# Kernel optimization log

Measured on AMD Instinct MI355X. Metric: run time of the kernel, lower is better.

## Reference

```python
import jax, jax.numpy as jnp
import numpy as np

MIN_NORM = 1e-15
BALL_EPS = 4e-3  # float32 proj eps used by HGCN PoincareBall
C_IN = 1.0
C_OUT = 1.0
N_NODES = 100000
N_EDGES = 1200000
DIM = 64
RATIO = 0.75


def _artanh(x):
    x = jnp.clip(x, -1.0 + 1e-7, 1.0 - 1e-7)
    return 0.5 * (jnp.log1p(x) - jnp.log1p(-x))


def _norm(x):
    return jnp.clip(jnp.linalg.norm(x, axis=-1, keepdims=True), MIN_NORM, None)


def proj(x, c):
    n = _norm(x)
    maxnorm = (1.0 - BALL_EPS) / jnp.sqrt(c)
    return jnp.where(n > maxnorm, x / n * maxnorm, x)


def expmap0(u, c):
    sc = jnp.sqrt(c)
    n = _norm(u)
    return jnp.tanh(sc * n) * u / (sc * n)


def logmap0(p, c):
    sc = jnp.sqrt(c)
    n = _norm(p)
    return _artanh(sc * n) * p / (sc * n)


def mobius_add(x, y, c):
    x2 = jnp.sum(x * x, -1, keepdims=True)
    y2 = jnp.sum(y * y, -1, keepdims=True)
    xy = jnp.sum(x * y, -1, keepdims=True)
    num = (1.0 + 2.0 * c * xy + c * y2) * x + (1.0 - c * x2) * y
    den = 1.0 + 2.0 * c * xy + c * c * x2 * y2
    return num / jnp.clip(den, MIN_NORM, None)


def mobius_matvec(m, x, c):
    sc = jnp.sqrt(c)
    xn = _norm(x)
    mx = x @ m.T  # [N, out]
    mxn = _norm(mx)
    res = jnp.tanh(mxn / xn * _artanh(sc * xn)) * mx / (mxn * sc)
    zero = jnp.all(mx == 0, axis=-1, keepdims=True)
    return jnp.where(zero, jnp.zeros((), mx.dtype), res)


def setup_inputs() -> dict:
    key = jax.random.key(0)
    k1, k2, k3, k4 = jax.random.split(key, 4)
    # points on the Poincare ball (small tangent vectors exp-mapped)
    x = proj(expmap0(0.01 * jax.random.normal(k1, (N_NODES, DIM), jnp.float32), C_IN), C_IN)
    edge_index = jax.random.randint(k2, (2, N_EDGES), 0, N_NODES, dtype=jnp.int32)
    xav = float(np.sqrt(2.0) * np.sqrt(6.0 / (DIM + DIM)))  # xavier_uniform gain sqrt(2) scale
    weight = jax.random.uniform(k3, (DIM, DIM), jnp.float32, -xav, xav)
    bias = jnp.zeros((DIM,), jnp.float32)
    lw_w = jax.random.normal(k4, (1, 2 * DIM), jnp.float32) * 0.05
    lw_b = jnp.zeros((1,), jnp.float32)
    return {"x": x, "edge_index": edge_index, "weight": weight, "bias": bias, "lw_w": lw_w, "lw_b": lw_b}


def reference(x, edge_index, weight, bias, lw_w, lw_b):
    N = x.shape[0]
    # ---- HypLinear (eval mode, dropout=0) ----
    h = proj(mobius_matvec(weight, x, C_IN), C_IN)
    hyp_bias = proj(expmap0(bias[None, :], C_IN), C_IN)  # proj_tan0 is identity on Poincare ball
    h = proj(mobius_add(h, hyp_bias, C_IN), C_IN)
    # ---- NodeSelect ----
    x_tan = logmap0(h, C_IN)  # [N, D]
    src, dst = edge_index[0], edge_index[1]
    agg = lambda v: jax.ops.segment_sum(v[src], dst, num_segments=N)  # scatter-add over edges
    sum_neigh = agg(x_tan)
    # NodeInformationScore: (I - D^{-1/2} A D^{-1/2}) x with self-loops removed from A
    w = (src != dst).astype(x_tan.dtype)
    deg = jax.ops.segment_sum(w, src, num_segments=N)
    dinv = jnp.where(deg > 0, deg ** -0.5, 0.0)
    norm_w = -(dinv[src] * w * dinv[dst])  # [E]
    info = x_tan + jax.ops.segment_sum(norm_w[:, None] * x_tan[src], dst, num_segments=N)
    score = jnp.sum(jnp.abs(info), axis=1)  # [N]
    k = int(N * RATIO)
    top_vals, _ = jax.lax.top_k(score, k)
    T = top_vals[k - 1]  # min of top-k
    sel = (score > T).astype(x_tan.dtype)[:, None]  # hot_prob mask [N,1]
    sum_sel = agg(sel * x_tan)
    gate = jax.nn.sigmoid(jnp.concatenate([sum_sel, sum_neigh], axis=-1) @ lw_w.T + lw_b)  # [N,1]
    a_x = jax.nn.relu(agg(gate * sel * x_tan))
    out = x_tan + a_x
    out = proj(expmap0(out, C_IN), C_IN)
    # ---- HypAct (relu) ----
    out = jax.nn.relu(out)
    out = proj(expmap0(out, C_OUT), C_OUT)
    return out
```

## Files before the change

kernel.cpp:

```cpp
#include <hip/hip_runtime.h>
#include <hip/hip_fp16.h>
#include <math.h>


#define MAXN_D 0.996
#define MAXN_F 0.996f
#define NPB 64
#define GPT 512
#define NBMAX 512
#define BCAP 6144
#define BINBLK 256
#define SELB 128
#define SBIN 8192
#define CAND_CAP 16384

typedef unsigned long long ull;

__device__ __forceinline__ double wsumd(double v){
#pragma unroll
  for(int o=32;o;o>>=1) v += __shfl_xor(v,o,64);
  return v;
}
__device__ __forceinline__ float wsumf(float v){
#pragma unroll
  for(int o=32;o;o>>=1) v += __shfl_xor(v,o,64);
  return v;
}
__device__ __forceinline__ float qsumf(float v){
#pragma unroll
  for(int o=1;o<16;o<<=1) v += __shfl_xor(v,o,64);
  return v;
}

__global__ __launch_bounds__(256) void k_init(
    const float* __restrict__ bias, double* __restrict__ hb,
    double* __restrict__ hb2, int* __restrict__ rem, int kth,
    int* __restrict__ dstCur, int* __restrict__ srcCur, int NB){
  if(threadIdx.x < 64){
    int lane = threadIdx.x;
    double b = (double)bias[lane];
    double n = fmax(sqrt(wsumd(b*b)), 1e-15);
    double e = tanh(n)*b/n;
    double en = fmax(sqrt(wsumd(e*e)), 1e-15);
    if(en > MAXN_D) e *= MAXN_D/en;
    hb[lane] = e;
    double s2 = wsumd(e*e);
    if(lane==0) *hb2 = s2;
  }
  if(threadIdx.x == 0) *rem = kth;
  for(int b=threadIdx.x; b<NB; b+=256){
    dstCur[b] = b*BCAP;
    srcCur[b] = b*BCAP;
  }
}

__global__ __launch_bounds__(256) void k_binPlace(const int* __restrict__ ei, int E,
    int NB, int chunk, int* __restrict__ dstCur, int* __restrict__ srcCur,
    ull* __restrict__ dstbin, int* __restrict__ srcbin){
  __shared__ int dh[NBMAX], sh_[NBMAX];
  __shared__ int db[NBMAX], sb[NBMAX];
  for(int t=threadIdx.x; t<NB; t+=256){ dh[t]=0; sh_[t]=0; }
  __syncthreads();
  int start = blockIdx.x*chunk, end = min(E, start+chunk);
  for(int e=start+(int)threadIdx.x; e<end; e+=256){
    int s = ei[e], d = ei[(size_t)E+e];
    atomicAdd(&dh[d>>8],1);
    if(s!=d) atomicAdd(&sh_[s>>8],1);
  }
  __syncthreads();
  for(int t=threadIdx.x; t<NB; t+=256){
    db[t] = dh[t]  ? atomicAdd(&dstCur[t], dh[t])  : 0;
    sb[t] = sh_[t] ? atomicAdd(&srcCur[t], sh_[t]) : 0;
  }
  __syncthreads();
  for(int t=threadIdx.x; t<NB; t+=256){ dh[t]=db[t]; sh_[t]=sb[t]; }
  __syncthreads();
  for(int e=start+(int)threadIdx.x; e<end; e+=256){
    int s = ei[e], d = ei[(size_t)E+e];
    int p = atomicAdd(&dh[d>>8],1);
    dstbin[p] = ((ull)(unsigned)d<<32) | (unsigned)s;
    if(s!=d){ int p2 = atomicAdd(&sh_[s>>8],1); srcbin[p2] = s; }
  }
}

__global__ __launch_bounds__(256) void k_bucketAB(
    const ull* __restrict__ dstbin, const int* __restrict__ dstCur,
    int* __restrict__ rowbeg, int* __restrict__ rowcnt, int* __restrict__ csr,
    const int* __restrict__ srcbin, const int* __restrict__ srcCur,
    double* __restrict__ dinv, int N){
  int b = blockIdx.x;
  int node0 = b<<8;
  int nodes = min(256, N-node0);
  __shared__ int c[256], ex[256];
  int t = threadIdx.x;
  {
    int base = b*BCAP, cnt = dstCur[b]-base;
    c[t]=0; __syncthreads();
    for(int e=base+t; e<base+cnt; e+=256){
      int d = (int)(dstbin[e]>>32);
      atomicAdd(&c[d-node0],1);
    }
    __syncthreads();
    int v = c[t]; ex[t]=v; __syncthreads();
    for(int off=1; off<256; off<<=1){
      int a = (t>=off) ? ex[t-off] : 0; __syncthreads();
      ex[t] += a; __syncthreads();
    }
    int mybase = base + ex[t] - v;
    if(t<nodes){ rowbeg[node0+t] = mybase; rowcnt[node0+t] = v; }
    c[t] = mybase;
    __syncthreads();
    for(int e=base+t; e<base+cnt; e+=256){
      ull pr = dstbin[e];
      int d = (int)(pr>>32);
      int p = atomicAdd(&c[d-node0],1);
      csr[p] = (int)(pr & 0xffffffffu);
    }
  }
  __syncthreads();
  {
    int base = b*BCAP, cnt = srcCur[b]-base;
    c[t]=0; __syncthreads();
    for(int e=base+t; e<base+cnt; e+=256)
      atomicAdd(&c[srcbin[e]-node0],1);
    __syncthreads();
    if(t<nodes){ int d = c[t]; dinv[node0+t] = (d>0) ? 1.0/sqrt((double)d) : 0.0; }
  }
}

__global__ __launch_bounds__(GPT) void k_gemmprep(
    const float* __restrict__ x, const float* __restrict__ W,
    const double* __restrict__ hb, const double* __restrict__ hb2p,
    const float* __restrict__ lww,
    float* __restrict__ xtf, float* __restrict__ xdl, __half* __restrict__ xth,
    float2* __restrict__ pab, int N){
  __shared__ float wf[4096];
  __shared__ float xf[NPB*64];
  __shared__ double r123[NPB][3];
  __shared__ double abuf[NPB][2];
  int tid = threadIdx.x;
  for(int a=tid; a<4096; a+=GPT){
    int j = (a>>2)&63;
    int k = ((a>>8)<<2) | (a&3);
    wf[a] = W[j*64 + k];
  }
  int i0 = blockIdx.x*NPB;
  for(int idx=tid; idx<NPB*64; idx+=GPT){
    int node = i0 + (idx>>6);
    xf[idx] = (node<N) ? x[(size_t)node*64 + (idx&63)] : 0.f;
  }
  __syncthreads();
  int lane = tid & 63;
  int nb = (tid>>6)*8;
  double acc0=0.0, acc1=0.0, acc2=0.0, acc3=0.0;
  double acc4=0.0, acc5=0.0, acc6=0.0, acc7=0.0;
  const float4* wq = (const float4*)wf;
  const float4* xq = (const float4*)xf;
#pragma unroll 2
  for(int k4=0; k4<16; ++k4){
    float4 w4 = wq[k4*64 + lane];
    double w0=(double)w4.x, w1=(double)w4.y, w2d=(double)w4.z, w3=(double)w4.w;
#define MAC(n, accn) { float4 v = xq[(nb+(n))*16 + k4];                       \
    accn = fma(w0,(double)v.x,accn); accn = fma(w1,(double)v.y,accn);         \
    accn = fma(w2d,(double)v.z,accn); accn = fma(w3,(double)v.w,accn); }
    MAC(0,acc0) MAC(1,acc1) MAC(2,acc2) MAC(3,acc3)
    MAC(4,acc4) MAC(5,acc5) MAC(6,acc6) MAC(7,acc7)
#undef MAC
  }
  double hbl = hb[lane];
#define RED4(A0,A1,A2,A3, OFF) {                                              \
    double xd0 = (double)xf[(nb+(OFF)+0)*64+lane];                            \
    double xd1 = (double)xf[(nb+(OFF)+1)*64+lane];                            \
    double xd2 = (double)xf[(nb+(OFF)+2)*64+lane];                            \
    double xd3 = (double)xf[(nb+(OFF)+3)*64+lane];                            \
    double s1_0 = wsumd(xd0*xd0), s2_0 = wsumd((A0)*(A0)), s3_0 = wsumd((A0)*hbl); \
    double s1_1 = wsumd(xd1*xd1), s2_1 = wsumd((A1)*(A1)), s3_1 = wsumd((A1)*hbl); \
    double s1_2 = wsumd(xd2*xd2), s2_2 = wsumd((A2)*(A2)), s3_2 = wsumd((A2)*hbl); \
    double s1_3 = wsumd(xd3*xd3), s2_3 = wsumd((A3)*(A3)), s3_3 = wsumd((A3)*hbl); \
    if(lane==0){                                                              \
      r123[nb+(OFF)+0][0]=s1_0; r123[nb+(OFF)+0][1]=s2_0; r123[nb+(OFF)+0][2]=s3_0; \
      r123[nb+(OFF)+1][0]=s1_1; r123[nb+(OFF)+1][1]=s2_1; r123[nb+(OFF)+1][2]=s3_1; \
      r123[nb+(OFF)+2][0]=s1_2; r123[nb+(OFF)+2][1]=s2_2; r123[nb+(OFF)+2][2]=s3_2; \
      r123[nb+(OFF)+3][0]=s1_3; r123[nb+(OFF)+3][1]=s2_3; r123[nb+(OFF)+3][2]=s3_3; \
    } }
  RED4(acc0,acc1,acc2,acc3, 0)
  RED4(acc4,acc5,acc6,acc7, 4)
#undef RED4
  __syncthreads();
  if(tid < 64){
    double x2s = r123[tid][0], m2 = r123[tid][1], mh = r123[tid][2];
    double y2 = *hb2p;
    double xn  = fmax(sqrt(x2s), 1e-15);
    double mxn = fmax(sqrt(m2), 1e-15);
    double xc  = fmin(fmax(xn, -1.0+1e-7), 1.0-1e-7);
    double at  = 0.5*(log1p(xc)-log1p(-xc));
    double f1  = tanh(mxn/xn*at)/mxn;
    if(m2 == 0.0) f1 = 0.0;
    double h2 = f1*f1*m2;
    double hn = fmax(sqrt(h2), 1e-15);
    if(hn > MAXN_D){ double s = MAXN_D/hn; f1 *= s; h2 = f1*f1*m2; }
    double xy = f1*mh;
    double den = fmax(1.0 + 2.0*xy + h2*y2, 1e-15);
    double a = (1.0 + 2.0*xy + y2)/den;
    double bb = (1.0 - h2)/den;
    double p2 = a*a*h2 + 2.0*a*bb*xy + bb*bb*y2;
    double pn = fmax(sqrt(p2), 1e-15);
    if(pn > MAXN_D){ double s = MAXN_D/pn; a*=s; bb*=s; pn = fmax(pn*s, 1e-15); }
    double nc  = fmin(fmax(pn, -1.0+1e-7), 1.0-1e-7);
    double at2 = 0.5*(log1p(nc)-log1p(-nc));
    double sc  = at2/pn;
    abuf[tid][0] = sc*a*f1;
    abuf[tid][1] = sc*bb;
  }
  __syncthreads();
  float wAl = lww[lane], wBl = lww[64+lane];
#define EMIT(n, accn) { int nd=i0+nb+(n); if(nd<N){                           \
    double al = abuf[nb+(n)][0], be = abuf[nb+(n)][1];                        \
    double v = al*(accn) + be*hbl;                                            \
    float vf = (float)v;                                                      \
    float df = (float)(v - (double)vf);                                       \
    xtf[(size_t)nd*64+lane] = vf;                                             \
    xdl[(size_t)nd*64+lane] = df;                                             \
    xth[(size_t)nd*64+lane] = __float2half(vf);                               \
    float pA = wsumf(vf*wAl);                                                 \
    float pB = wsumf(vf*wBl);                                                 \
    if(lane==0) pab[nd] = make_float2(pA,pB); } }
  EMIT(0,acc0) EMIT(1,acc1) EMIT(2,acc2) EMIT(3,acc3)
  EMIT(4,acc4) EMIT(5,acc5) EMIT(6,acc6) EMIT(7,acc7)
#undef EMIT
}

__global__ void k_gatherA(const int* __restrict__ csr, const int* __restrict__ rowbeg,
                          const int* __restrict__ rowcnt,
                          const float* __restrict__ xtf, const float* __restrict__ xdl,
                          const double* __restrict__ dinv,
                          ull* __restrict__ keys, int N){
  int lane = threadIdx.x & 63;
  int i = (int)((blockIdx.x*(unsigned)blockDim.x + threadIdx.x)>>6);
  if(i>=N) return;
  int beg = rowbeg[i], deg = rowcnt[i];
  int g = lane>>3, t = lane&7;
  double di = dinv[i];
  double a0=0,a1=0,a2=0,a3=0,a4=0,a5=0,a6=0,a7=0;
  int j = g;
  int s = (j<deg) ? csr[beg+j] : 0;
  while(j < deg){
    int snext = (j+8<deg) ? csr[beg+j+8] : 0;
    if(s != i){
      double w = di*dinv[s];
      const float4* row = (const float4*)(xtf + (size_t)s*64 + t*8);
      float4 u = row[0], v = row[1];
      a0 -= w*(double)u.x; a1 -= w*(double)u.y; a2 -= w*(double)u.z; a3 -= w*(double)u.w;
      a4 -= w*(double)v.x; a5 -= w*(double)v.y; a6 -= w*(double)v.z; a7 -= w*(double)v.w;
    }
    s = snext; j += 8;
  }
#define XG(v) { v += __shfl_xor(v,8,64); v += __shfl_xor(v,16,64); v += __shfl_xor(v,32,64); }
  XG(a0) XG(a1) XG(a2) XG(a3) XG(a4) XG(a5) XG(a6) XG(a7)
#undef XG
  const float4* xr = (const float4*)(xtf + (size_t)i*64 + t*8);
  const float4* dr = (const float4*)(xdl + (size_t)i*64 + t*8);
  float4 x0 = xr[0], x1 = xr[1], d0 = dr[0], d1 = dr[1];
  double sc =
    fabs(((double)x0.x+(double)d0.x)+a0) + fabs(((double)x0.y+(double)d0.y)+a1) +
    fabs(((double)x0.z+(double)d0.z)+a2) + fabs(((double)x0.w+(double)d0.w)+a3) +
    fabs(((double)x1.x+(double)d1.x)+a4) + fabs(((double)x1.y+(double)d1.y)+a5) +
    fabs(((double)x1.z+(double)d1.z)+a6) + fabs(((double)x1.w+(double)d1.w)+a7);
  sc += __shfl_xor(sc,1,64); sc += __shfl_xor(sc,2,64); sc += __shfl_xor(sc,4,64);
  if(lane==0) keys[i] = (ull)__double_as_longlong(sc);
}

__global__ __launch_bounds__(256) void k_sel13(
    const ull* __restrict__ keys, int N,
    ull* __restrict__ pref, int* __restrict__ rem,
    int lev, int shift, int width,
    int* __restrict__ hist , int* __restrict__ ticket){
  __shared__ int h[SBIN];
  __shared__ int part[256];
  __shared__ int lastflag, pickedD, pickedR;
  int t = threadIdx.x;
  for(int b=t; b<SBIN; b+=256) h[b] = 0;
  __syncthreads();
  ull p0 = *pref;
  int rem0 = *rem;
  int mask = (1<<width) - 1;
  for(int i = blockIdx.x*256 + t; i<N; i += SELB*256){
    ull kk = keys[i];
    if(lev==0 || (kk >> (shift+width)) == (p0 >> (shift+width)))
      atomicAdd(&h[(int)((kk>>shift)&mask)], 1);
  }
  __syncthreads();
  for(int b=t; b<SBIN; b+=256)
    if(h[b]) __hip_atomic_fetch_add(&hist[b], h[b],
                                    __ATOMIC_RELAXED, __HIP_MEMORY_SCOPE_AGENT);
  __threadfence();
  if(t==0){
    int tk = __hip_atomic_fetch_add(ticket, 1, __ATOMIC_ACQ_REL, __HIP_MEMORY_SCOPE_AGENT);
    lastflag = (tk == SELB-1);
  }
  __syncthreads();
  if(!lastflag) return;
  int base = SBIN-1 - 32*t;
  int pt = 0;
  for(int m=0;m<32;m++)
    pt += __hip_atomic_load(&hist[base-m], __ATOMIC_RELAXED, __HIP_MEMORY_SCOPE_AGENT);
  part[t] = pt;
  __syncthreads();
  for(int off=1; off<256; off<<=1){
    int a = (t>=off) ? part[t-off] : 0; __syncthreads();
    part[t] += a; __syncthreads();
  }
  int cumt = part[t];
  int prev = (t==0) ? 0 : part[t-1];
  if(cumt >= rem0 && prev < rem0){
    int c = 0;
    for(int m=0;m<32;m++){
      int hv = __hip_atomic_load(&hist[base-m], __ATOMIC_RELAXED, __HIP_MEMORY_SCOPE_AGENT);
      c += hv;
      if(prev + c >= rem0){ pickedD = base-m; pickedR = rem0 - (prev + c - hv); break; }
    }
  }
  __syncthreads();
  if(t==0){
    *rem = pickedR;
    *pref = p0 | ((ull)pickedD << shift);
  }
}

__global__ __launch_bounds__(256) void k_finish(
    const ull* __restrict__ keys, int N,
    ull* __restrict__ pref, const int* __restrict__ rem,
    ull* __restrict__ cand, int* __restrict__ cnt, int* __restrict__ ticket){
  __shared__ ull sc[4096];
  __shared__ int lastflag;
  __shared__ ull winner;
  int t = threadIdx.x;
  ull p0 = *pref;
  for(int i = blockIdx.x*256 + t; i<N; i += SELB*256){
    ull kk = keys[i];
    if((kk>>38) == (p0>>38)){
      int idx = __hip_atomic_fetch_add(cnt, 1, __ATOMIC_RELAXED, __HIP_MEMORY_SCOPE_AGENT);
      if(idx < CAND_CAP)
        __hip_atomic_store(&cand[idx], kk, __ATOMIC_RELAXED, __HIP_MEMORY_SCOPE_AGENT);
    }
  }
  __threadfence();
  __syncthreads();
  if(t==0){
    int tk = __hip_atomic_fetch_add(ticket, 1, __ATOMIC_ACQ_REL, __HIP_MEMORY_SCOPE_AGENT);
    lastflag = (tk == SELB-1);
  }
  __syncthreads();
  if(!lastflag) return;
  int C = __hip_atomic_load(cnt, __ATOMIC_RELAXED, __HIP_MEMORY_SCOPE_AGENT);
  if(C > 4096) C = 4096;
  for(int j=t; j<C; j+=256)
    sc[j] = __hip_atomic_load(&cand[j], __ATOMIC_RELAXED, __HIP_MEMORY_SCOPE_AGENT);
  __syncthreads();
  int r = *rem;
  for(int j=t; j<C; j+=256){
    ull c = sc[j];
    int gt=0, eq=0;
    for(int m=0;m<C;m++){ ull o = sc[m]; gt += (o>c); eq += (o==c); }
    if(gt <= r-1 && r-1 < gt+eq) winner = c;
  }
  __syncthreads();
  if(t==0) *pref = winner;
}

__global__ void k_qval(const float2* __restrict__ pab, const ull* __restrict__ keys,
                       const ull* __restrict__ pref, float* __restrict__ q, int N){
  int i = blockIdx.x*blockDim.x + threadIdx.x;
  if(i>=N) return;
  float2 p = pab[i];
  q[i] = p.y + ((keys[i] > *pref) ? p.x : 0.f);
}

__global__ void k_gatherC(const int* __restrict__ csr, const int* __restrict__ rowbeg,
                          const int* __restrict__ rowcnt,
                          const float* __restrict__ q,
                          const ull* __restrict__ keys, const ull* __restrict__ pref,
                          const float* __restrict__ lwb,
                          float* __restrict__ gg, int N){
  int lane = threadIdx.x & 63;
  int wid  = (int)((blockIdx.x*(unsigned)blockDim.x + threadIdx.x)>>6);
  int g = lane>>4, t = lane&15;
  int i = wid*4 + g;
  if(i>=N) return;
  int beg = rowbeg[i], end = beg + rowcnt[i];
  float z = 0.f;
  for(int e = beg + t; e < end; e += 16) z += q[csr[e]];
  z = qsumf(z);
  if(t==0){
    float gv = 1.f/(1.f+expf(-(z + lwb[0])));
    gg[i] = (keys[i] > *pref) ? gv : 0.f;
  }
}

__global__ void k_gatherD(const int* __restrict__ csr, const int* __restrict__ rowbeg,
                          const int* __restrict__ rowcnt,
                          const float* __restrict__ xtf, const __half* __restrict__ xth,
                          const float* __restrict__ gg,
                          float* __restrict__ out, int N){
  int lane = threadIdx.x & 63;
  int i = (int)((blockIdx.x*(unsigned)blockDim.x + threadIdx.x)>>6);
  if(i>=N) return;
  int beg = rowbeg[i], deg = rowcnt[i];
  int g = lane>>3, t = lane&7;
  float c0=0,c1=0,c2=0,c3=0,c4=0,c5=0,c6=0,c7=0;
  int j = g;
  int s = (j<deg) ? csr[beg+j] : 0;
  while(j < deg){
    int snext = (j+8<deg) ? csr[beg+j+8] : 0;
    float gv = gg[s];
    if(gv != 0.f){
      float4 raw = *(const float4*)(xth + (size_t)s*64 + t*8);
      const __half2* hp = (const __half2*)&raw;
      float2 p0 = __half22float2(hp[0]);
      float2 p1 = __half22float2(hp[1]);
      float2 p2 = __half22float2(hp[2]);
      float2 p3 = __half22float2(hp[3]);
      c0 = fmaf(gv,p0.x,c0); c1 = fmaf(gv,p0.y,c1); c2 = fmaf(gv,p1.x,c2); c3 = fmaf(gv,p1.y,c3);
      c4 = fmaf(gv,p2.x,c4); c5 = fmaf(gv,p2.y,c5); c6 = fmaf(gv,p3.x,c6); c7 = fmaf(gv,p3.y,c7);
    }
    s = snext; j += 8;
  }
#define XG(v) { v += __shfl_xor(v,8,64); v += __shfl_xor(v,16,64); v += __shfl_xor(v,32,64); }
  XG(c0) XG(c1) XG(c2) XG(c3) XG(c4) XG(c5) XG(c6) XG(c7)
#undef XG
  const float4* xr = (const float4*)(xtf + (size_t)i*64 + t*8);
  float4 x0 = xr[0], x1 = xr[1];
  float v0 = x0.x + fmaxf(c0,0.f), v1 = x0.y + fmaxf(c1,0.f);
  float v2 = x0.z + fmaxf(c2,0.f), v3 = x0.w + fmaxf(c3,0.f);
  float v4 = x1.x + fmaxf(c4,0.f), v5 = x1.y + fmaxf(c5,0.f);
  float v6 = x1.z + fmaxf(c6,0.f), v7 = x1.w + fmaxf(c7,0.f);
  float n2 = v0*v0+v1*v1+v2*v2+v3*v3+v4*v4+v5*v5+v6*v6+v7*v7;
  n2 += __shfl_xor(n2,1,64); n2 += __shfl_xor(n2,2,64); n2 += __shfl_xor(n2,4,64);
  float n = fmaxf(sqrtf(n2), 1e-15f);
  float f = tanhf(n)/n;
  float e0=f*v0,e1=f*v1,e2=f*v2,e3=f*v3,e4=f*v4,e5=f*v5,e6=f*v6,e7=f*v7;
  float en = fmaxf(tanhf(n), 1e-15f);
  if(en > MAXN_F){ float sf = MAXN_F/en;
    e0*=sf;e1*=sf;e2*=sf;e3*=sf;e4*=sf;e5*=sf;e6*=sf;e7*=sf; }
  e0=fmaxf(e0,0.f);e1=fmaxf(e1,0.f);e2=fmaxf(e2,0.f);e3=fmaxf(e3,0.f);
  e4=fmaxf(e4,0.f);e5=fmaxf(e5,0.f);e6=fmaxf(e6,0.f);e7=fmaxf(e7,0.f);
  float m2 = e0*e0+e1*e1+e2*e2+e3*e3+e4*e4+e5*e5+e6*e6+e7*e7;
  m2 += __shfl_xor(m2,1,64); m2 += __shfl_xor(m2,2,64); m2 += __shfl_xor(m2,4,64);
  float nb = fmaxf(sqrtf(m2), 1e-15f);
  float f2 = tanhf(nb)/nb;
  float o0=f2*e0,o1=f2*e1,o2=f2*e2,o3=f2*e3,o4=f2*e4,o5=f2*e5,o6=f2*e6,o7=f2*e7;
  float on = fmaxf(tanhf(nb), 1e-15f);
  if(on > MAXN_F){ float sf = MAXN_F/on;
    o0*=sf;o1*=sf;o2*=sf;o3*=sf;o4*=sf;o5*=sf;o6*=sf;o7*=sf; }
  if(g==0){
    float4* op = (float4*)(out + (size_t)i*64 + t*8);
    op[0] = make_float4(o0,o1,o2,o3);
    op[1] = make_float4(o4,o5,o6,o7);
  }
}

extern "C" void kernel_launch(void* const* d_in, const int* in_sizes, int n_in,
                              void* d_out, int out_size, void* d_ws, size_t ws_size,
                              hipStream_t stream){
  const float* x    = (const float*)d_in[0];
  const int*   ei   = (const int*)d_in[1];
  const float* W    = (const float*)d_in[2];
  const float* bias = (const float*)d_in[3];
  const float* lww  = (const float*)d_in[4];
  const float* lwb  = (const float*)d_in[5];
  int N = in_sizes[0]/64;
  int E = in_sizes[1]/2;
  int kth = (int)((double)N*0.75);
  int NB = (N+255)>>8;
  if(NB > NBMAX) return;
  long long meanPB = (long long)E / (NB > 0 ? NB : 1);
  if(3*meanPB > 2*(long long)BCAP) return;
  int chunk = (E + BINBLK - 1)/BINBLK;
  size_t binEls = (size_t)NB*BCAP + 4096;

  char* ws = (char*)d_ws;
  size_t cur = 0;
  auto alloc = [&](size_t bytes){ size_t o = cur; cur = (cur + bytes + 255) & ~(size_t)255; return o; };
  size_t o_hb   = alloc(64*sizeof(double));
  size_t o_hb2  = alloc(8);
  size_t o_rem  = alloc(4);
  size_t o_zero = cur;
  size_t o_pref = alloc(8);
  size_t o_hist = alloc(2*(size_t)SBIN*4);
  size_t o_tick = alloc(3*4);
  size_t o_cnt  = alloc(4);
  size_t zlen   = cur - o_zero;
  size_t o_cand = alloc((size_t)CAND_CAP*8);
  size_t o_dCur = alloc((size_t)NBMAX*4);
  size_t o_sCur = alloc((size_t)NBMAX*4);
  size_t o_rbeg = alloc((size_t)N*4);
  size_t o_rcnt = alloc((size_t)N*4);
  size_t o_csr  = alloc(binEls*4);
  size_t o_dbin = alloc(binEls*8);
  size_t o_sbin = alloc(binEls*4);
  size_t o_dinv = alloc((size_t)N*8);
  size_t o_keys = alloc((size_t)N*8);
  size_t o_pab  = alloc((size_t)N*8);
  size_t o_q    = alloc((size_t)N*4);
  size_t o_xtf  = alloc((size_t)N*64*4);
  size_t o_xdl  = alloc((size_t)N*64*4);
  size_t o_xth  = alloc((size_t)N*64*2);
  size_t o_gg   = alloc((size_t)N*4);
  if(ws_size < cur) return;

  double* hb     = (double*)(ws+o_hb);
  double* hb2    = (double*)(ws+o_hb2);
  int*    rem    = (int*)(ws+o_rem);
  ull*    pref   = (ull*)(ws+o_pref);
  int*    hist   = (int*)(ws+o_hist);
  int*    tick   = (int*)(ws+o_tick);
  int*    cnt    = (int*)(ws+o_cnt);
  ull*    cand   = (ull*)(ws+o_cand);
  int*    dstCur = (int*)(ws+o_dCur);
  int*    srcCur = (int*)(ws+o_sCur);
  int*    rowbeg = (int*)(ws+o_rbeg);
  int*    rowcnt = (int*)(ws+o_rcnt);
  int*    csr    = (int*)(ws+o_csr);
  ull*    dstbin = (ull*)(ws+o_dbin);
  int*    srcbin = (int*)(ws+o_sbin);
  double* dinv   = (double*)(ws+o_dinv);
  ull*    keys   = (ull*)(ws+o_keys);
  float2* pab    = (float2*)(ws+o_pab);
  float*  q      = (float*)(ws+o_q);
  float*  xtf    = (float*)(ws+o_xtf);
  float*  xdl    = (float*)(ws+o_xdl);
  __half* xth    = (__half*)(ws+o_xth);
  float*  gg     = (float*)(ws+o_gg);

  hipMemsetAsync(ws+o_zero, 0, zlen, stream);

  int nodeBlocks = (N+3)/4;
  int pBlocks    = (N+15)/16;

  k_init     <<<1, 256, 0, stream>>>(bias, hb, hb2, rem, kth, dstCur, srcCur, NB);
  k_binPlace <<<BINBLK, 256, 0, stream>>>(ei, E, NB, chunk, dstCur, srcCur, dstbin, srcbin);
  k_bucketAB <<<NB, 256, 0, stream>>>(dstbin, dstCur, rowbeg, rowcnt, csr,
                                      srcbin, srcCur, dinv, N);
  k_gemmprep <<<(N+NPB-1)/NPB, GPT, 0, stream>>>(x, W, hb, hb2, lww, xtf, xdl, xth, pab, N);
  k_gatherA  <<<nodeBlocks, 256, 0, stream>>>(csr, rowbeg, rowcnt, xtf, xdl, dinv, keys, N);
  k_sel13    <<<SELB, 256, 0, stream>>>(keys, N, pref, rem, 0, 51, 13, hist, tick+0);
  k_sel13    <<<SELB, 256, 0, stream>>>(keys, N, pref, rem, 1, 38, 13, hist+SBIN, tick+1);
  k_finish   <<<SELB, 256, 0, stream>>>(keys, N, pref, rem, cand, cnt, tick+2);
  k_qval     <<<(N+255)/256, 256, 0, stream>>>(pab, keys, pref, q, N);
  k_gatherC  <<<pBlocks, 256, 0, stream>>>(csr, rowbeg, rowcnt, q, keys, pref, lwb, gg, N);
  k_gatherD  <<<nodeBlocks, 256, 0, stream>>>(csr, rowbeg, rowcnt, xtf, xth, gg, (float*)d_out, N);
}
```

Before: 338.2 us.

## Merge edge binning and GEMM prep into one launch via block specialization

The edge-binning kernel and the HypLinear GEMM/prep kernel are independent, so they are merged into a single launch. The first blocks do binning and the rest do the GEMM. Both share one statically sized shared memory buffer, and binning now runs with 512 threads per block. This removes one launch and lets the memory-bound binning overlap the compute-heavy GEMM. The cost is that the binning blocks carry the GEMM's shared-memory footprint, which may limit occupancy.

```diff
diff --git a/kernel.cpp b/kernel.cpp
--- a/kernel.cpp
+++ b/kernel.cpp
@@ -54,97 +54,58 @@
   }
 }
 
-__global__ __launch_bounds__(256) void k_binPlace(const int* __restrict__ ei, int E,
-    int NB, int chunk, int* __restrict__ dstCur, int* __restrict__ srcCur,
-    ull* __restrict__ dstbin, int* __restrict__ srcbin){
-  __shared__ int dh[NBMAX], sh_[NBMAX];
-  __shared__ int db[NBMAX], sb[NBMAX];
-  for(int t=threadIdx.x; t<NB; t+=256){ dh[t]=0; sh_[t]=0; }
-  __syncthreads();
-  int start = blockIdx.x*chunk, end = min(E, start+chunk);
-  for(int e=start+(int)threadIdx.x; e<end; e+=256){
-    int s = ei[e], d = ei[(size_t)E+e];
-    atomicAdd(&dh[d>>8],1);
-    if(s!=d) atomicAdd(&sh_[s>>8],1);
-  }
-  __syncthreads();
-  for(int t=threadIdx.x; t<NB; t+=256){
-    db[t] = dh[t]  ? atomicAdd(&dstCur[t], dh[t])  : 0;
-    sb[t] = sh_[t] ? atomicAdd(&srcCur[t], sh_[t]) : 0;
-  }
-  __syncthreads();
-  for(int t=threadIdx.x; t<NB; t+=256){ dh[t]=db[t]; sh_[t]=sb[t]; }
-  __syncthreads();
-  for(int e=start+(int)threadIdx.x; e<end; e+=256){
-    int s = ei[e], d = ei[(size_t)E+e];
-    int p = atomicAdd(&dh[d>>8],1);
-    dstbin[p] = ((ull)(unsigned)d<<32) | (unsigned)s;
-    if(s!=d){ int p2 = atomicAdd(&sh_[s>>8],1); srcbin[p2] = s; }
-  }
-}
-
-__global__ __launch_bounds__(256) void k_bucketAB(
-    const ull* __restrict__ dstbin, const int* __restrict__ dstCur,
-    int* __restrict__ rowbeg, int* __restrict__ rowcnt, int* __restrict__ csr,
-    const int* __restrict__ srcbin, const int* __restrict__ srcCur,
-    double* __restrict__ dinv, int N){
-  int b = blockIdx.x;
-  int node0 = b<<8;
-  int nodes = min(256, N-node0);
-  __shared__ int c[256], ex[256];
-  int t = threadIdx.x;
-  {
-    int base = b*BCAP, cnt = dstCur[b]-base;
-    c[t]=0; __syncthreads();
-    for(int e=base+t; e<base+cnt; e+=256){
-      int d = (int)(dstbin[e]>>32);
-      atomicAdd(&c[d-node0],1);
-    }
-    __syncthreads();
-    int v = c[t]; ex[t]=v; __syncthreads();
-    for(int off=1; off<256; off<<=1){
-      int a = (t>=off) ? ex[t-off] : 0; __syncthreads();
-      ex[t] += a; __syncthreads();
-    }
-    int mybase = base + ex[t] - v;
-    if(t<nodes){ rowbeg[node0+t] = mybase; rowcnt[node0+t] = v; }
-    c[t] = mybase;
-    __syncthreads();
-    for(int e=base+t; e<base+cnt; e+=256){
-      ull pr = dstbin[e];
-      int d = (int)(pr>>32);
-      int p = atomicAdd(&c[d-node0],1);
-      csr[p] = (int)(pr & 0xffffffffu);
-    }
-  }
-  __syncthreads();
-  {
-    int base = b*BCAP, cnt = srcCur[b]-base;
-    c[t]=0; __syncthreads();
-    for(int e=base+t; e<base+cnt; e+=256)
-      atomicAdd(&c[srcbin[e]-node0],1);
-    __syncthreads();
-    if(t<nodes){ int d = c[t]; dinv[node0+t] = (d>0) ? 1.0/sqrt((double)d) : 0.0; }
-  }
-}
-
-__global__ __launch_bounds__(GPT) void k_gemmprep(
+__global__ __launch_bounds__(GPT) void k_fat(
+    const int* __restrict__ ei, int E, int NB, int chunk,
+    int* __restrict__ dstCur, int* __restrict__ srcCur,
+    ull* __restrict__ dstbin, int* __restrict__ srcbin, int binBlocks,
     const float* __restrict__ x, const float* __restrict__ W,
     const double* __restrict__ hb, const double* __restrict__ hb2p,
     const float* __restrict__ lww,
     float* __restrict__ xtf, float* __restrict__ xdl, __half* __restrict__ xth,
     float2* __restrict__ pab, int N){
-  __shared__ float wf[4096];
-  __shared__ float xf[NPB*64];
-  __shared__ double r123[NPB][3];
-  __shared__ double abuf[NPB][2];
+  __shared__ __align__(16) char smem[35328];
   int tid = threadIdx.x;
+
+  if(blockIdx.x < (unsigned)binBlocks){
+    int* dh  = (int*)smem;
+    int* sh_ = (int*)(smem + 2048);
+    int* db  = (int*)(smem + 4096);
+    int* sb  = (int*)(smem + 6144);
+    for(int t=tid; t<NB; t+=GPT){ dh[t]=0; sh_[t]=0; }
+    __syncthreads();
+    int start = blockIdx.x*chunk, end = min(E, start+chunk);
+    for(int e=start+tid; e<end; e+=GPT){
+      int s = ei[e], d = ei[(size_t)E+e];
+      atomicAdd(&dh[d>>8],1);
+      if(s!=d) atomicAdd(&sh_[s>>8],1);
+    }
+    __syncthreads();
+    for(int t=tid; t<NB; t+=GPT){
+      db[t] = dh[t]  ? atomicAdd(&dstCur[t], dh[t])  : 0;
+      sb[t] = sh_[t] ? atomicAdd(&srcCur[t], sh_[t]) : 0;
+    }
+    __syncthreads();
+    for(int t=tid; t<NB; t+=GPT){ dh[t]=db[t]; sh_[t]=sb[t]; }
+    __syncthreads();
+    for(int e=start+tid; e<end; e+=GPT){
+      int s = ei[e], d = ei[(size_t)E+e];
+      int p = atomicAdd(&dh[d>>8],1);
+      dstbin[p] = ((ull)(unsigned)d<<32) | (unsigned)s;
+      if(s!=d){ int p2 = atomicAdd(&sh_[s>>8],1); srcbin[p2] = s; }
+    }
+    return;
+  }
+
+  float*  wf   = (float*)smem;
+  float*  xf   = (float*)(smem + 16384);
+  double (*r123)[3] = (double(*)[3])(smem + 32768);
+  double (*abuf)[2] = (double(*)[2])(smem + 34304);
   for(int a=tid; a<4096; a+=GPT){
     int j = (a>>2)&63;
     int k = ((a>>8)<<2) | (a&3);
     wf[a] = W[j*64 + k];
   }
-  int i0 = blockIdx.x*NPB;
+  int i0 = (blockIdx.x - binBlocks)*NPB;
   for(int idx=tid; idx<NPB*64; idx+=GPT){
     int node = i0 + (idx>>6);
     xf[idx] = (node<N) ? x[(size_t)node*64 + (idx&63)] : 0.f;
@@ -228,6 +189,51 @@
   EMIT(0,acc0) EMIT(1,acc1) EMIT(2,acc2) EMIT(3,acc3)
   EMIT(4,acc4) EMIT(5,acc5) EMIT(6,acc6) EMIT(7,acc7)
 #undef EMIT
+}
+
+__global__ __launch_bounds__(256) void k_bucketAB(
+    const ull* __restrict__ dstbin, const int* __restrict__ dstCur,
+    int* __restrict__ rowbeg, int* __restrict__ rowcnt, int* __restrict__ csr,
+    const int* __restrict__ srcbin, const int* __restrict__ srcCur,
+    double* __restrict__ dinv, int N){
+  int b = blockIdx.x;
+  int node0 = b<<8;
+  int nodes = min(256, N-node0);
+  __shared__ int c[256], ex[256];
+  int t = threadIdx.x;
+  {
+    int base = b*BCAP, cnt = dstCur[b]-base;
+    c[t]=0; __syncthreads();
+    for(int e=base+t; e<base+cnt; e+=256){
+      int d = (int)(dstbin[e]>>32);
+      atomicAdd(&c[d-node0],1);
+    }
+    __syncthreads();
+    int v = c[t]; ex[t]=v; __syncthreads();
+    for(int off=1; off<256; off<<=1){
+      int a = (t>=off) ? ex[t-off] : 0; __syncthreads();
+      ex[t] += a; __syncthreads();
+    }
+    int mybase = base + ex[t] - v;
+    if(t<nodes){ rowbeg[node0+t] = mybase; rowcnt[node0+t] = v; }
+    c[t] = mybase;
+    __syncthreads();
+    for(int e=base+t; e<base+cnt; e+=256){
+      ull pr = dstbin[e];
+      int d = (int)(pr>>32);
+      int p = atomicAdd(&c[d-node0],1);
+      csr[p] = (int)(pr & 0xffffffffu);
+    }
+  }
+  __syncthreads();
+  {
+    int base = b*BCAP, cnt = srcCur[b]-base;
+    c[t]=0; __syncthreads();
+    for(int e=base+t; e<base+cnt; e+=256)
+      atomicAdd(&c[srcbin[e]-node0],1);
+    __syncthreads();
+    if(t<nodes){ int d = c[t]; dinv[node0+t] = (d>0) ? 1.0/sqrt((double)d) : 0.0; }
+  }
 }
 
 __global__ void k_gatherA(const int* __restrict__ csr, const int* __restrict__ rowbeg,
@@ -536,12 +542,14 @@
 
   int nodeBlocks = (N+3)/4;
   int pBlocks    = (N+15)/16;
+  int gpBlocks   = (N+NPB-1)/NPB;
 
   k_init     <<<1, 256, 0, stream>>>(bias, hb, hb2, rem, kth, dstCur, srcCur, NB);
-  k_binPlace <<<BINBLK, 256, 0, stream>>>(ei, E, NB, chunk, dstCur, srcCur, dstbin, srcbin);
+  k_fat      <<<BINBLK + gpBlocks, GPT, 0, stream>>>(
+                 ei, E, NB, chunk, dstCur, srcCur, dstbin, srcbin, BINBLK,
+                 x, W, hb, hb2, lww, xtf, xdl, xth, pab, N);
   k_bucketAB <<<NB, 256, 0, stream>>>(dstbin, dstCur, rowbeg, rowcnt, csr,
                                       srcbin, srcCur, dinv, N);
-  k_gemmprep <<<(N+NPB-1)/NPB, GPT, 0, stream>>>(x, W, hb, hb2, lww, xtf, xdl, xth, pab, N);
   k_gatherA  <<<nodeBlocks, 256, 0, stream>>>(csr, rowbeg, rowcnt, xtf, xdl, dinv, keys, N);
   k_sel13    <<<SELB, 256, 0, stream>>>(keys, N, pref, rem, 0, 51, 13, hist, tick+0);
   k_sel13    <<<SELB, 256, 0, stream>>>(keys, N, pref, rem, 1, 38, 13, hist+SBIN, tick+1);
```

Result: faster. 318.0 us (median of 2 runs) (-6.0%).
